# Optimization experiments

Measured on AMD Instinct MI355X. Metric: run time of the kernel, lower is better.

Reference implementation:

```python
import jax, jax.numpy as jnp
import numpy as np

N_NODES = 50000
N_EDGES = 800000
D_IN = 256
D_H = 128
D_OUT = 2
NUM_FC = 2


def setup_inputs() -> dict:
    key = jax.random.key(0)
    ks = jax.random.split(key, 12)
    s = 0.05
    inp = {
        "x": jax.random.normal(ks[0], (N_NODES, D_IN), dtype=jnp.float32),
        "edge_index": jax.random.randint(ks[1], (2, N_EDGES), 0, N_NODES, dtype=jnp.int64),
        "W_gcn": jax.random.normal(ks[2], (D_IN, D_H), dtype=jnp.float32) * s,
        "b_gcn": jnp.zeros((D_H,), dtype=jnp.float32),
        "fc1_W": jax.random.normal(ks[3], (D_H, D_H), dtype=jnp.float32) * s,
        "fc1_b": jnp.zeros((D_H,), dtype=jnp.float32),
        "fc2_W": jax.random.normal(ks[4], (D_H, D_H), dtype=jnp.float32) * s,
        "fc2_b": jnp.zeros((D_H,), dtype=jnp.float32),
        "out_W": jax.random.normal(ks[5], (D_H, D_OUT), dtype=jnp.float32) * s,
        "out_b": jnp.zeros((D_OUT,), dtype=jnp.float32),
    }
    return inp


def _gcn_conv(x, edge_index, W, b):
    # PyG GCNConv: add self-loops, symmetric normalization D^-1/2 (A+I) D^-1/2, then aggregate X@W.
    n = x.shape[0]
    loops = jnp.arange(n, dtype=edge_index.dtype)
    src = jnp.concatenate([edge_index[0], loops])
    dst = jnp.concatenate([edge_index[1], loops])
    h = x @ W  # [N, D_H]
    deg = jax.ops.segment_sum(jnp.ones_like(dst, dtype=h.dtype), dst, num_segments=n)
    dinv = jnp.where(deg > 0, jax.lax.rsqrt(deg), 0.0)
    norm = dinv[src] * dinv[dst]  # [E+N]
    msg = h[src] * norm[:, None]
    out = jax.ops.segment_sum(msg, dst, num_segments=n)
    return out + b


def _mlp_stack(h, fc1_W, fc1_b, fc2_W, fc2_b):
    # fc -> relu (dropout is eval-mode identity)
    h = jax.nn.relu(h @ fc1_W + fc1_b)
    h = jax.nn.relu(h @ fc2_W + fc2_b)
    return h


def reference(x, edge_index, W_gcn, b_gcn, fc1_W, fc1_b, fc2_W, fc2_b, out_W, out_b):
    h = jax.nn.relu(_gcn_conv(x, edge_index, W_gcn, b_gcn))  # [N, D_H]
    h = _mlp_stack(h, fc1_W, fc1_b, fc2_W, fc2_b)
    # edge-pair gather + average
    edge_x = (h[edge_index[0]] + h[edge_index[1]]) * 0.5  # [E, D_H]
    # note: same fc weights reused, faithful to source
    edge_x = _mlp_stack(edge_x, fc1_W, fc1_b, fc2_W, fc2_b)
    scores = edge_x @ out_W + out_b  # [E, D_OUT]
    return jax.nn.log_softmax(scores, axis=1)
```

## Files before the change

kernel.cpp:

```cpp
#include <hip/hip_runtime.h>

#define NN 50000
#define NE 800000
#define DIN 256
#define DH 128
#define BCAP 64

typedef float f32x4 __attribute__((ext_vector_type(4)));
typedef __bf16 bf16x8 __attribute__((ext_vector_type(8)));
typedef unsigned short u16;
typedef unsigned int u32;

__device__ __forceinline__ u16 f2b(float f) { return __builtin_bit_cast(u16, (__bf16)f); }
__device__ __forceinline__ float lo_f(u32 u) { return (float)__builtin_bit_cast(__bf16, (u16)(u & 0xFFFFu)); }
__device__ __forceinline__ float hi_f(u32 u) { return (float)__builtin_bit_cast(__bf16, (u16)(u >> 16)); }

__device__ __forceinline__ f32x4 mfma16(bf16x8 a, bf16x8 b, f32x4 c) {
    return __builtin_amdgcn_mfma_f32_16x16x32_bf16(a, b, c, 0, 0, 0);
}

__global__ void k_prep_fill(const float* __restrict__ w1, const float* __restrict__ w2,
                            const float* __restrict__ wg,
                            u16* __restrict__ w12f, u16* __restrict__ wgf,
                            const int* __restrict__ ei,
                            int* __restrict__ cnt, int* __restrict__ bucket) {
    int b = blockIdx.x;
    if (b < 32) {
        int t = b * 256 + threadIdx.x;
        const float* src; u16* dst; int id;
        if (t < 2048)      { src = w1; dst = w12f;          id = t; }
        else if (t < 4096) { src = w2; dst = w12f + 16384;  id = t - 2048; }
        else               { src = wg; dst = wgf;           id = t - 4096; }
        int lane = id & 63, frag = id >> 6;
        int kt = frag >> 3, nt = frag & 7;
        int k0 = kt * 32 + (lane >> 4) * 8, n = nt * 16 + (lane & 15);
        u16 v[8];
#pragma unroll
        for (int j = 0; j < 8; ++j) v[j] = f2b(src[(k0 + j) * 128 + n]);
#pragma unroll
        for (int j = 0; j < 8; ++j) dst[id * 8 + j] = v[j];
    } else {
        int e = (b - 32) * 256 + threadIdx.x;
        int d = ei[NE + e];
        int pos = atomicAdd(&cnt[d], 1);
        bucket[d * BCAP + pos] = ei[e];
    }
}

__global__ __launch_bounds__(128) void k_gemm_x(const float* __restrict__ x,
                                                const u16* __restrict__ wgf,
                                                const int* __restrict__ cnt,
                                                u16* __restrict__ h0pre) {
    int wave = threadIdx.x >> 6, lane = threadIdx.x & 63;
    int l15 = lane & 15, q = lane >> 4;
    int rowBase = blockIdx.x * 64 + wave * 32;

    bf16x8 a[2][8];
#pragma unroll
    for (int mi = 0; mi < 2; ++mi) {
        int r = rowBase + mi * 16 + l15; if (r >= NN) r = NN - 1;
        const float* rp = x + (size_t)r * DIN + q * 8;
#pragma unroll
        for (int kt = 0; kt < 8; ++kt) {
            f32x4 f0 = *(const f32x4*)(rp + kt * 32);
            f32x4 f1 = *(const f32x4*)(rp + kt * 32 + 4);
            bf16x8 aa;
#pragma unroll
            for (int j = 0; j < 4; ++j) { aa[j] = (__bf16)f0[j]; aa[j + 4] = (__bf16)f1[j]; }
            a[mi][kt] = aa;
        }
    }
    f32x4 z = {0.f, 0.f, 0.f, 0.f};
    f32x4 acc[2][8];
#pragma unroll
    for (int mi = 0; mi < 2; ++mi)
#pragma unroll
        for (int nt = 0; nt < 8; ++nt) acc[mi][nt] = z;

#pragma unroll
    for (int kt = 0; kt < 8; ++kt)
#pragma unroll
        for (int nt = 0; nt < 8; ++nt) {
            bf16x8 b = *(const bf16x8*)(wgf + ((kt * 8 + nt) * 64 + lane) * 8);
            acc[0][nt] = mfma16(a[0][kt], b, acc[0][nt]);
            acc[1][nt] = mfma16(a[1][kt], b, acc[1][nt]);
        }
#pragma unroll
    for (int mi = 0; mi < 2; ++mi)
#pragma unroll
        for (int rg = 0; rg < 4; ++rg) {
            int r = rowBase + mi * 16 + q * 4 + rg;
            if (r < NN) {
                float dv = rsqrtf((float)cnt[r] + 1.0f);
#pragma unroll
                for (int nt = 0; nt < 8; ++nt)
                    h0pre[r * DH + nt * 16 + l15] = f2b(acc[mi][nt][rg] * dv);
            }
        }
}

__global__ __launch_bounds__(256) void k_aggregate(const u16* __restrict__ h0pre,
                                                   const int* __restrict__ cnt,
                                                   const int* __restrict__ bucket,
                                                   const float* __restrict__ bg,
                                                   u16* __restrict__ hA) {
    int wave = threadIdx.x >> 6, lane = threadIdx.x & 63;
    int hw = lane >> 5, l32 = lane & 31;
    int v = blockIdx.x * 8 + wave * 2 + hw;
    const uint2* h2p = (const uint2*)h0pre;

    uint2 su = h2p[v * 32 + l32];
    float a0[4], a1[4], a2[4], a3[4];
#pragma unroll
    for (int k = 0; k < 4; ++k) { a0[k] = 0.f; a1[k] = 0.f; a2[k] = 0.f; a3[k] = 0.f; }
    a0[0] = lo_f(su.x); a1[0] = hi_f(su.x); a2[0] = lo_f(su.y); a3[0] = hi_f(su.y);

    int deg = cnt[v];
    const int* bk = bucket + v * BCAP;
    int j = 0;
    for (; j + 8 <= deg; j += 8) {
        int idx[8]; uint2 u[8];
#pragma unroll
        for (int k = 0; k < 8; ++k) idx[k] = bk[j + k];
#pragma unroll
        for (int k = 0; k < 8; ++k) u[k] = h2p[idx[k] * 32 + l32];
#pragma unroll
        for (int k = 0; k < 8; ++k) {
            a0[k & 3] += lo_f(u[k].x); a1[k & 3] += hi_f(u[k].x);
            a2[k & 3] += lo_f(u[k].y); a3[k & 3] += hi_f(u[k].y);
        }
    }
    for (; j + 2 <= deg; j += 2) {
        uint2 ua = h2p[bk[j] * 32 + l32];
        uint2 ub = h2p[bk[j + 1] * 32 + l32];
        a0[0] += lo_f(ua.x); a1[0] += hi_f(ua.x); a2[0] += lo_f(ua.y); a3[0] += hi_f(ua.y);
        a0[1] += lo_f(ub.x); a1[1] += hi_f(ub.x); a2[1] += lo_f(ub.y); a3[1] += hi_f(ub.y);
    }
    for (; j < deg; ++j) {
        uint2 u = h2p[bk[j] * 32 + l32];
        a0[0] += lo_f(u.x); a1[0] += hi_f(u.x); a2[0] += lo_f(u.y); a3[0] += hi_f(u.y);
    }
    float r0 = (a0[0] + a0[1]) + (a0[2] + a0[3]);
    float r1 = (a1[0] + a1[1]) + (a1[2] + a1[3]);
    float r2 = (a2[0] + a2[1]) + (a2[2] + a2[3]);
    float r3 = (a3[0] + a3[1]) + (a3[2] + a3[3]);
    float dv = rsqrtf((float)deg + 1.0f);
    float4 bgv = ((const float4*)bg)[l32];
    r0 = fmaxf(r0 * dv + bgv.x, 0.f);
    r1 = fmaxf(r1 * dv + bgv.y, 0.f);
    r2 = fmaxf(r2 * dv + bgv.z, 0.f);
    r3 = fmaxf(r3 * dv + bgv.w, 0.f);
    uint2 outw;
    outw.x = (u32)f2b(r0) | ((u32)f2b(r1) << 16);
    outw.y = (u32)f2b(r2) | ((u32)f2b(r3) << 16);
    ((uint2*)hA)[v * 32 + l32] = outw;
}

__global__ __launch_bounds__(256) void k_node_mlp(const u16* __restrict__ hA,
                                                  const u16* __restrict__ wf,
                                                  const float* __restrict__ b1,
                                                  const float* __restrict__ b2,
                                                  u16* __restrict__ gh) {
    __shared__ __align__(16) u16 wlds[16384];
    __shared__ __align__(16) u16 sct[4][2176];
    {
        const uint4* s = (const uint4*)wf;
        uint4* d = (uint4*)wlds;
        for (int i = threadIdx.x; i < 2048; i += 256) d[i] = s[i];
    }
    __syncthreads();
    int wave = threadIdx.x >> 6, lane = threadIdx.x & 63;
    int l15 = lane & 15, q = lane >> 4;
    int rowBase = blockIdx.x * 128 + wave * 32;
    u16* sw = sct[wave];

    bf16x8 a[2][4];
#pragma unroll
    for (int mi = 0; mi < 2; ++mi) {
        int r = rowBase + mi * 16 + l15; if (r >= NN) r = NN - 1;
        const u16* rp = hA + r * DH + q * 8;
#pragma unroll
        for (int kt = 0; kt < 4; ++kt) a[mi][kt] = *(const bf16x8*)(rp + kt * 32);
    }
    f32x4 z = {0.f, 0.f, 0.f, 0.f};
    f32x4 acc1[2][8];
#pragma unroll
    for (int mi = 0; mi < 2; ++mi)
#pragma unroll
        for (int nt = 0; nt < 8; ++nt) acc1[mi][nt] = z;
#pragma unroll
    for (int kt = 0; kt < 4; ++kt)
#pragma unroll
        for (int nt = 0; nt < 8; ++nt) {
            bf16x8 b = *(const bf16x8*)(wlds + (kt * 8 + nt) * 512 + lane * 8);
            acc1[0][nt] = mfma16(a[0][kt], b, acc1[0][nt]);
            acc1[1][nt] = mfma16(a[1][kt], b, acc1[1][nt]);
        }
    float bb1[8], bb2[8];
#pragma unroll
    for (int nt = 0; nt < 8; ++nt) { bb1[nt] = b1[nt * 16 + l15]; bb2[nt] = b2[nt * 16 + l15]; }

    bf16x8 a2[2][4];
#pragma unroll
    for (int mi = 0; mi < 2; ++mi) {
#pragma unroll
        for (int nt = 0; nt < 8; ++nt)
#pragma unroll
            for (int rg = 0; rg < 4; ++rg) {
                float v = acc1[mi][nt][rg] + bb1[nt];
                v = v > 0.f ? v : 0.f;
                sw[(q * 4 + rg) * 136 + nt * 16 + l15] = f2b(v);
            }
#pragma unroll
        for (int kt = 0; kt < 4; ++kt)
            a2[mi][kt] = *(const bf16x8*)(sw + l15 * 136 + kt * 32 + q * 8);
    }
    __syncthreads();
    {
        const uint4* s = (const uint4*)(wf + 16384);
        uint4* d = (uint4*)wlds;
        for (int i = threadIdx.x; i < 2048; i += 256) d[i] = s[i];
    }
    __syncthreads();
    f32x4 acc2[2][8];
#pragma unroll
    for (int mi = 0; mi < 2; ++mi)
#pragma unroll
        for (int nt = 0; nt < 8; ++nt) acc2[mi][nt] = z;
#pragma unroll
    for (int kt = 0; kt < 4; ++kt)
#pragma unroll
        for (int nt = 0; nt < 8; ++nt) {
            bf16x8 b = *(const bf16x8*)(wlds + (kt * 8 + nt) * 512 + lane * 8);
            acc2[0][nt] = mfma16(a2[0][kt], b, acc2[0][nt]);
            acc2[1][nt] = mfma16(a2[1][kt], b, acc2[1][nt]);
        }
    bf16x8 a3[2][4];
#pragma unroll
    for (int mi = 0; mi < 2; ++mi) {
#pragma unroll
        for (int nt = 0; nt < 8; ++nt)
#pragma unroll
            for (int rg = 0; rg < 4; ++rg) {
                float v = acc2[mi][nt][rg] + bb2[nt];
                v = v > 0.f ? v : 0.f;
                sw[(q * 4 + rg) * 136 + nt * 16 + l15] = f2b(v);
            }
#pragma unroll
        for (int kt = 0; kt < 4; ++kt)
            a3[mi][kt] = *(const bf16x8*)(sw + l15 * 136 + kt * 32 + q * 8);
    }
    __syncthreads();
    {
        const uint4* s = (const uint4*)wf;
        uint4* d = (uint4*)wlds;
        for (int i = threadIdx.x; i < 2048; i += 256) d[i] = s[i];
    }
    __syncthreads();
    f32x4 acc3[2][8];
#pragma unroll
    for (int mi = 0; mi < 2; ++mi)
#pragma unroll
        for (int nt = 0; nt < 8; ++nt) acc3[mi][nt] = z;
#pragma unroll
    for (int kt = 0; kt < 4; ++kt)
#pragma unroll
        for (int nt = 0; nt < 8; ++nt) {
            bf16x8 b = *(const bf16x8*)(wlds + (kt * 8 + nt) * 512 + lane * 8);
            acc3[0][nt] = mfma16(a3[0][kt], b, acc3[0][nt]);
            acc3[1][nt] = mfma16(a3[1][kt], b, acc3[1][nt]);
        }
#pragma unroll
    for (int mi = 0; mi < 2; ++mi)
#pragma unroll
        for (int nt = 0; nt < 8; ++nt)
#pragma unroll
            for (int rg = 0; rg < 4; ++rg) {
                int r = rowBase + mi * 16 + q * 4 + rg;
                if (r < NN)
                    gh[r * DH + nt * 16 + l15] = f2b(0.5f * acc3[mi][nt][rg] + 0.5f * bb1[nt]);
            }
}

__global__ __launch_bounds__(256, 3) void k_edge_mlp(const u16* __restrict__ gh,
                                                     const int* __restrict__ ei,
                                                     const u16* __restrict__ wf,
                                                     const float* __restrict__ b2,
                                                     const float* __restrict__ ow,
                                                     const float* __restrict__ ob,
                                                     float2* __restrict__ outp) {
    __shared__ __align__(16) u16 wlds[16384];
    {
        const uint4* s = (const uint4*)(wf + 16384);
        uint4* d = (uint4*)wlds;
        for (int i = threadIdx.x; i < 2048; i += 256) d[i] = s[i];
    }
    int wave = threadIdx.x >> 6, lane = threadIdx.x & 63;
    int l15 = lane & 15, q = lane >> 4;
    int eBase = blockIdx.x * 256 + wave * 64;

    int se[4], de[4];
#pragma unroll
    for (int ti = 0; ti < 4; ++ti) {
        int e = eBase + ti * 16 + l15;
        se[ti] = ei[e];
        de[ti] = ei[NE + e];
    }
    bf16x8 gsA[4], gdA[4], gsB[4], gdB[4];
    {
        const u16* ps = gh + se[0] * DH + q * 8;
        const u16* pd = gh + de[0] * DH + q * 8;
#pragma unroll
        for (int kt = 0; kt < 4; ++kt) {
            gsA[kt] = *(const bf16x8*)(ps + kt * 32);
            gdA[kt] = *(const bf16x8*)(pd + kt * 32);
        }
    }
    {
        const u16* ps = gh + se[1] * DH + q * 8;
        const u16* pd = gh + de[1] * DH + q * 8;
#pragma unroll
        for (int kt = 0; kt < 4; ++kt) {
            gsB[kt] = *(const bf16x8*)(ps + kt * 32);
            gdB[kt] = *(const bf16x8*)(pd + kt * 32);
        }
    }
    float bb2[8], owp0[8], owp1[8];
#pragma unroll
    for (int nt = 0; nt < 8; ++nt) {
        int k = nt * 16 + l15;
        bb2[nt] = b2[k];
        owp0[nt] = ow[2 * k];
        owp1[nt] = ow[2 * k + 1];
    }
    float ob0 = ob[0], ob1 = ob[1];
    __syncthreads();
    f32x4 z = {0.f, 0.f, 0.f, 0.f};

#pragma unroll
    for (int ti = 0; ti < 4; ++ti) {
        bf16x8 fs[4], fd[4];
#pragma unroll
        for (int kt = 0; kt < 4; ++kt) {
            fs[kt] = (ti & 1) ? gsB[kt] : gsA[kt];
            fd[kt] = (ti & 1) ? gdB[kt] : gdA[kt];
        }
        if (ti + 2 < 4) {
            const u16* ps = gh + se[ti + 2] * DH + q * 8;
            const u16* pd = gh + de[ti + 2] * DH + q * 8;
#pragma unroll
            for (int kt = 0; kt < 4; ++kt) {
                if (ti & 1) { gsB[kt] = *(const bf16x8*)(ps + kt * 32); gdB[kt] = *(const bf16x8*)(pd + kt * 32); }
                else        { gsA[kt] = *(const bf16x8*)(ps + kt * 32); gdA[kt] = *(const bf16x8*)(pd + kt * 32); }
            }
        }
        bf16x8 a2[4];
#pragma unroll
        for (int kt = 0; kt < 4; ++kt) {
            bf16x8 r;
#pragma unroll
            for (int j = 0; j < 8; ++j) {
                float t = (float)fs[kt][j] + (float)fd[kt][j];
                r[j] = (__bf16)(t > 0.f ? t : 0.f);
            }
            a2[kt] = r;
        }
        f32x4 acc2[8];
#pragma unroll
        for (int nt = 0; nt < 8; ++nt) acc2[nt] = z;
#pragma unroll
        for (int kt = 0; kt < 4; ++kt)
#pragma unroll
            for (int nt = 0; nt < 8; ++nt) {
                bf16x8 b = *(const bf16x8*)(wlds + (kt * 8 + nt) * 512 + lane * 8);
                acc2[nt] = mfma16(a2[kt], b, acc2[nt]);
            }
#pragma unroll
        for (int rg = 0; rg < 4; ++rg) {
            float p0 = 0.f, p1 = 0.f;
#pragma unroll
            for (int nt = 0; nt < 8; ++nt) {
                float t = acc2[nt][rg] + bb2[nt];
                t = t > 0.f ? t : 0.f;
                p0 += t * owp0[nt];
                p1 += t * owp1[nt];
            }
#pragma unroll
            for (int m = 1; m < 16; m <<= 1) {
                p0 += __shfl_xor(p0, m, 64);
                p1 += __shfl_xor(p1, m, 64);
            }
            if (l15 == 0) {
                int e = eBase + ti * 16 + q * 4 + rg;
                float s0 = p0 + ob0, s1 = p1 + ob1;
                float mx = fmaxf(s0, s1);
                float lse = mx + __logf(__expf(s0 - mx) + __expf(s1 - mx));
                outp[e] = make_float2(s0 - lse, s1 - lse);
            }
        }
    }
}

extern "C" void kernel_launch(void* const* d_in, const int* in_sizes, int n_in,
                              void* d_out, int out_size, void* d_ws, size_t ws_size,
                              hipStream_t stream) {
    const float* x  = (const float*)d_in[0];
    const int* ei   = (const int*)d_in[1];
    const float* wg = (const float*)d_in[2];
    const float* bg = (const float*)d_in[3];
    const float* w1 = (const float*)d_in[4];
    const float* b1 = (const float*)d_in[5];
    const float* w2 = (const float*)d_in[6];
    const float* b2 = (const float*)d_in[7];
    const float* ow = (const float*)d_in[8];
    const float* ob = (const float*)d_in[9];
    float2* out = (float2*)d_out;

    char* ws = (char*)d_ws;
    size_t off = 0;
    auto alloc = [&](size_t bytes) { void* p = ws + off; off += (bytes + 255) & ~(size_t)255; return p; };
    u16* h0      = (u16*)alloc((size_t)NN * DH * 2);
    u16* hA      = (u16*)alloc((size_t)NN * DH * 2);
    int* bucket  = (int*)alloc((size_t)NN * BCAP * 4);
    int* cnt     = (int*)alloc((size_t)NN * 4);
    u16* w12f    = (u16*)alloc(65536);
    u16* wgf     = (u16*)alloc(65536);
    u16* gh      = h0;

    hipMemsetAsync(cnt, 0, (size_t)NN * 4, stream);
    k_prep_fill<<<32 + NE / 256, 256, 0, stream>>>(w1, w2, wg, w12f, wgf, ei, cnt, bucket);
    k_gemm_x<<<(NN + 63) / 64, 128, 0, stream>>>(x, wgf, cnt, h0);
    k_aggregate<<<NN / 8, 256, 0, stream>>>(h0, cnt, bucket, bg, hA);
    k_node_mlp<<<(NN + 127) / 128, 256, 0, stream>>>(hA, w12f, b1, b2, gh);
    k_edge_mlp<<<NE / 256, 256, 0, stream>>>(gh, ei, w12f, b2, ow, ob, out);
}
```

Measured before the change: 302.2 us.

## Process two edge tiles per MFMA pass in edge MLP, share LDS weight loads

The edge MLP kernel now handles two 16-edge tiles at a time, so each LDS weight fragment feeds two MFMAs instead of one and LDS traffic per edge is halved. The bf16 add+relu conversion uses bit-shift unpacking into packed float pairs rather than per-element casts. Register pressure rises from two accumulator sets, so launch bounds drop from 3 to 2 blocks per SM, which may reduce occupancy and the latency hiding available for the irregular gathers.

```diff
diff --git a/kernel.cpp b/kernel.cpp
--- a/kernel.cpp
+++ b/kernel.cpp
@@ -7,9 +7,11 @@
 #define BCAP 64
 
 typedef float f32x4 __attribute__((ext_vector_type(4)));
+typedef float f32x2 __attribute__((ext_vector_type(2)));
 typedef __bf16 bf16x8 __attribute__((ext_vector_type(8)));
 typedef unsigned short u16;
 typedef unsigned int u32;
+typedef u32 u32x4 __attribute__((ext_vector_type(4)));
 
 __device__ __forceinline__ u16 f2b(float f) { return __builtin_bit_cast(u16, (__bf16)f); }
 __device__ __forceinline__ float lo_f(u32 u) { return (float)__builtin_bit_cast(__bf16, (u16)(u & 0xFFFFu)); }
@@ -282,7 +284,7 @@
             }
 }
 
-__global__ __launch_bounds__(256, 3) void k_edge_mlp(const u16* __restrict__ gh,
+__global__ __launch_bounds__(256, 2) void k_edge_mlp(const u16* __restrict__ gh,
                                                      const int* __restrict__ ei,
                                                      const u16* __restrict__ wf,
                                                      const float* __restrict__ b2,
@@ -306,25 +308,72 @@
         se[ti] = ei[e];
         de[ti] = ei[NE + e];
     }
-    bf16x8 gsA[4], gdA[4], gsB[4], gdB[4];
-    {
-        const u16* ps = gh + se[0] * DH + q * 8;
-        const u16* pd = gh + de[0] * DH + q * 8;
-#pragma unroll
-        for (int kt = 0; kt < 4; ++kt) {
-            gsA[kt] = *(const bf16x8*)(ps + kt * 32);
-            gdA[kt] = *(const bf16x8*)(pd + kt * 32);
-        }
-    }
-    {
-        const u16* ps = gh + se[1] * DH + q * 8;
-        const u16* pd = gh + de[1] * DH + q * 8;
-#pragma unroll
-        for (int kt = 0; kt < 4; ++kt) {
-            gsB[kt] = *(const bf16x8*)(ps + kt * 32);
-            gdB[kt] = *(const bf16x8*)(pd + kt * 32);
-        }
-    }
+
+#define LOADT(ti, S, D)                                         \
+    {                                                           \
+        const u16* ps = gh + se[ti] * DH + q * 8;               \
+        const u16* pd = gh + de[ti] * DH + q * 8;               \
+        _Pragma("unroll")                                       \
+        for (int kt = 0; kt < 4; ++kt) {                        \
+            S[kt] = *(const bf16x8*)(ps + kt * 32);             \
+            D[kt] = *(const bf16x8*)(pd + kt * 32);             \
+        }                                                       \
+    }
+
+#define CONV(A, S, D)                                                        \
+    {                                                                        \
+        _Pragma("unroll")                                                    \
+        for (int kt = 0; kt < 4; ++kt) {                                     \
+            u32x4 su = __builtin_bit_cast(u32x4, S[kt]);                     \
+            u32x4 du = __builtin_bit_cast(u32x4, D[kt]);                     \
+            u32x4 ou;                                                        \
+            _Pragma("unroll")                                                \
+            for (int j = 0; j < 4; ++j) {                                    \
+                f32x2 sv, dv;                                                \
+                sv.x = __builtin_bit_cast(float, su[j] << 16);               \
+                sv.y = __builtin_bit_cast(float, su[j] & 0xffff0000u);       \
+                dv.x = __builtin_bit_cast(float, du[j] << 16);               \
+                dv.y = __builtin_bit_cast(float, du[j] & 0xffff0000u);       \
+                f32x2 tv = sv + dv;                                          \
+                tv.x = tv.x > 0.f ? tv.x : 0.f;                              \
+                tv.y = tv.y > 0.f ? tv.y : 0.f;                              \
+                ou[j] = (u32)f2b(tv.x) | ((u32)f2b(tv.y) << 16);             \
+            }                                                                \
+            A[kt] = __builtin_bit_cast(bf16x8, ou);                          \
+        }                                                                    \
+    }
+
+#define EPI(ACC, ti)                                                         \
+    {                                                                        \
+        _Pragma("unroll")                                                    \
+        for (int rg = 0; rg < 4; ++rg) {                                     \
+            float p0 = 0.f, p1 = 0.f;                                        \
+            _Pragma("unroll")                                                \
+            for (int nt = 0; nt < 8; ++nt) {                                 \
+                float t = ACC[nt][rg] + bb2[nt];                             \
+                t = t > 0.f ? t : 0.f;                                       \
+                p0 += t * owp0[nt];                                          \
+                p1 += t * owp1[nt];                                          \
+            }                                                                \
+            _Pragma("unroll")                                                \
+            for (int m = 1; m < 16; m <<= 1) {                               \
+                p0 += __shfl_xor(p0, m, 64);                                 \
+                p1 += __shfl_xor(p1, m, 64);                                 \
+            }                                                                \
+            if (l15 == 0) {                                                  \
+                int e = eBase + (ti) * 16 + q * 4 + rg;                      \
+                float sc0 = p0 + ob0, sc1 = p1 + ob1;                        \
+                float mx = fmaxf(sc0, sc1);                                  \
+                float lse = mx + __logf(__expf(sc0 - mx) + __expf(sc1 - mx)); \
+                outp[e] = make_float2(sc0 - lse, sc1 - lse);                 \
+            }                                                                \
+        }                                                                    \
+    }
+
+    bf16x8 s0[4], d0[4], s1[4], d1[4];
+    LOADT(0, s0, d0);
+    LOADT(1, s1, d1);
+
     float bb2[8], owp0[8], owp1[8];
 #pragma unroll
     for (int nt = 0; nt < 8; ++nt) {
@@ -337,68 +386,49 @@
     __syncthreads();
     f32x4 z = {0.f, 0.f, 0.f, 0.f};
 
-#pragma unroll
-    for (int ti = 0; ti < 4; ++ti) {
-        bf16x8 fs[4], fd[4];
-#pragma unroll
-        for (int kt = 0; kt < 4; ++kt) {
-            fs[kt] = (ti & 1) ? gsB[kt] : gsA[kt];
-            fd[kt] = (ti & 1) ? gdB[kt] : gdA[kt];
-        }
-        if (ti + 2 < 4) {
-            const u16* ps = gh + se[ti + 2] * DH + q * 8;
-            const u16* pd = gh + de[ti + 2] * DH + q * 8;
-#pragma unroll
-            for (int kt = 0; kt < 4; ++kt) {
-                if (ti & 1) { gsB[kt] = *(const bf16x8*)(ps + kt * 32); gdB[kt] = *(const bf16x8*)(pd + kt * 32); }
-                else        { gsA[kt] = *(const bf16x8*)(ps + kt * 32); gdA[kt] = *(const bf16x8*)(pd + kt * 32); }
-            }
-        }
-        bf16x8 a2[4];
-#pragma unroll
-        for (int kt = 0; kt < 4; ++kt) {
-            bf16x8 r;
-#pragma unroll
-            for (int j = 0; j < 8; ++j) {
-                float t = (float)fs[kt][j] + (float)fd[kt][j];
-                r[j] = (__bf16)(t > 0.f ? t : 0.f);
-            }
-            a2[kt] = r;
-        }
-        f32x4 acc2[8];
-#pragma unroll
-        for (int nt = 0; nt < 8; ++nt) acc2[nt] = z;
+    {
+        bf16x8 a20[4], a21[4];
+        CONV(a20, s0, d0);
+        LOADT(2, s0, d0);
+        CONV(a21, s1, d1);
+        LOADT(3, s1, d1);
+
+        f32x4 acc0[8], acc1[8];
+#pragma unroll
+        for (int nt = 0; nt < 8; ++nt) { acc0[nt] = z; acc1[nt] = z; }
 #pragma unroll
         for (int kt = 0; kt < 4; ++kt)
 #pragma unroll
             for (int nt = 0; nt < 8; ++nt) {
                 bf16x8 b = *(const bf16x8*)(wlds + (kt * 8 + nt) * 512 + lane * 8);
-                acc2[nt] = mfma16(a2[kt], b, acc2[nt]);
-            }
-#pragma unroll
-        for (int rg = 0; rg < 4; ++rg) {
-            float p0 = 0.f, p1 = 0.f;
+                acc0[nt] = mfma16(a20[kt], b, acc0[nt]);
+                acc1[nt] = mfma16(a21[kt], b, acc1[nt]);
+            }
+        EPI(acc0, 0);
+        EPI(acc1, 1);
+    }
+    {
+        bf16x8 a20[4], a21[4];
+        CONV(a20, s0, d0);
+        CONV(a21, s1, d1);
+
+        f32x4 acc0[8], acc1[8];
+#pragma unroll
+        for (int nt = 0; nt < 8; ++nt) { acc0[nt] = z; acc1[nt] = z; }
+#pragma unroll
+        for (int kt = 0; kt < 4; ++kt)
 #pragma unroll
             for (int nt = 0; nt < 8; ++nt) {
-                float t = acc2[nt][rg] + bb2[nt];
-                t = t > 0.f ? t : 0.f;
-                p0 += t * owp0[nt];
-                p1 += t * owp1[nt];
-            }
-#pragma unroll
-            for (int m = 1; m < 16; m <<= 1) {
-                p0 += __shfl_xor(p0, m, 64);
-                p1 += __shfl_xor(p1, m, 64);
-            }
-            if (l15 == 0) {
-                int e = eBase + ti * 16 + q * 4 + rg;
-                float s0 = p0 + ob0, s1 = p1 + ob1;
-                float mx = fmaxf(s0, s1);
-                float lse = mx + __logf(__expf(s0 - mx) + __expf(s1 - mx));
-                outp[e] = make_float2(s0 - lse, s1 - lse);
-            }
-        }
-    }
+                bf16x8 b = *(const bf16x8*)(wlds + (kt * 8 + nt) * 512 + lane * 8);
+                acc0[nt] = mfma16(a20[kt], b, acc0[nt]);
+                acc1[nt] = mfma16(a21[kt], b, acc1[nt]);
+            }
+        EPI(acc0, 2);
+        EPI(acc1, 3);
+    }
+#undef LOADT
+#undef CONV
+#undef EPI
 }
 
 extern "C" void kernel_launch(void* const* d_in, const int* in_sizes, int n_in,
```

Result: slower. 310.5 us (+2.8%).
